# Optimization experiments

Hardware: AMD Instinct MI355X
Metric: run time of the kernel (lower is better)

Reference implementation:

```python
import jax, jax.numpy as jnp
import numpy as np

N_ATOMS = 2048
N_METAL = 512
BOX = (20.0, 20.0, 40.0)   # orthorhombic slab cell (A)
DL = 2.0                    # EwaldPotential dl -> k-grid half-extent per dim
SIGMA = 0.5540037           # 1/1.805132, Gaussian charge width
NMAX = tuple(int(np.ceil(L / DL)) for L in BOX)


def _kgrid():
    # integer reciprocal-lattice grid, k=0 excluded (built once at trace time)
    nx, ny, nz = NMAX
    g = np.stack(np.meshgrid(np.arange(-nx, nx + 1),
                             np.arange(-ny, ny + 1),
                             np.arange(-nz, nz + 1), indexing='ij'), -1).reshape(-1, 3)
    g = g[np.any(g != 0, axis=1)]
    return g.astype(np.float32)

_GRID = _kgrid()  # [K,3]


def ewald_field(r, q, cell):
    """Reciprocal-space Ewald potential phi_i = dE/dq_i for Gaussian-smeared charges.
    r:[N,3] q:[N,C] cell:[3,3] (rows = lattice vectors). Returns [N,C]."""
    V = jnp.abs(jnp.linalg.det(cell))
    recip = 2.0 * jnp.pi * jnp.linalg.inv(cell).T          # rows: reciprocal vectors
    k = jnp.asarray(_GRID, dtype=r.dtype) @ recip          # [K,3]
    k2 = jnp.sum(k * k, axis=-1)                           # [K]
    kfac = jnp.exp(-0.5 * SIGMA * SIGMA * k2) / k2         # exponent=1 kernel
    phase = r @ k.T                                        # [N,K]  (dominant traffic)
    c, s = jnp.cos(phase), jnp.sin(phase)
    cq = kfac[:, None] * (c.T @ q)                         # [K,C]
    sq = kfac[:, None] * (s.T @ q)
    return (4.0 * jnp.pi / V) * (c @ cq + s @ sq)          # [N,C]


def setup_inputs() -> dict:
    key = jax.random.key(0)
    k1, k2 = jax.random.split(key)
    box = jnp.asarray(BOX, dtype=jnp.float32)
    positions = jax.random.uniform(k1, (N_ATOMS, 3), dtype=jnp.float32) * box
    q = jax.random.normal(k2, (N_ATOMS, 1), dtype=jnp.float32) * 0.5
    cell = jnp.diag(box)
    # metal (Z=79) atoms occupy the first N_METAL slots; rest electrolyte (Z=8)
    atomic_numbers = jnp.concatenate([
        jnp.full((N_METAL,), 79, dtype=jnp.int32),
        jnp.full((N_ATOMS - N_METAL,), 8, dtype=jnp.int32)])
    return {"positions": positions, "q": q, "cell": cell,
            "atomic_numbers": atomic_numbers, "n_metal": N_METAL}


def reference(positions, q, cell, atomic_numbers, n_metal):
    nm = int(n_metal)  # static: metal atoms are the first nm rows
    dt = positions.dtype
    # q_all[metal] = 0
    q = q.at[:nm].set(0.0)
    # capacitance matrix S from detached coords (torch uses r.detach(), cell.detach())
    r_m = jax.lax.stop_gradient(positions[:nm])
    cell_d = jax.lax.stop_gradient(cell)
    A = ewald_field(r_m, jnp.eye(nm, dtype=dt), cell_d)     # [nm,nm] A_mat
    A_inv = jnp.linalg.inv(A)
    ones = jnp.ones((nm, 1), dtype=dt)
    Ai1 = A_inv @ ones                                       # [nm,1]
    S = A_inv - (Ai1 @ Ai1.T) / (ones.T @ Ai1)               # charge-neutral projector
    # full-system field; scaling_factor=1, external_field=None -> B_ext = 0
    f = ewald_field(positions, q, cell)                      # [N,1]
    B = -f[:nm]
    q_mw = q.at[:nm].set(S @ B)
    e_corr = jnp.zeros((1,), dtype=dt)   # scaling_factor == 1.0 branch
    e_ext = jnp.zeros((1,), dtype=dt)    # external_field is None
    return q_mw, e_corr, e_ext
```

## Files before the change

kernel.cpp:

```cpp
#include <hip/hip_runtime.h>
#include <math.h>

#define N_ATOMS 2048
#define NM      512
#define KHALF   9040
#define KPAD    9216
#define TWO_PI  6.2831853071795864769f
#define SIGMA   0.5540037f
#define FOUR_PI 12.566370614359172954f

__device__ inline void inv3x3(const float* __restrict__ c, float inv[3][3], float& det) {
    float a00=c[0],a01=c[1],a02=c[2],a10=c[3],a11=c[4],a12=c[5],a20=c[6],a21=c[7],a22=c[8];
    float c00 =  a11*a22 - a12*a21;
    float c01 = -(a10*a22 - a12*a20);
    float c02 =  a10*a21 - a11*a20;
    det = a00*c00 + a01*c01 + a02*c02;
    float id = 1.0f/det;
    inv[0][0] = c00*id;
    inv[0][1] = -(a01*a22 - a02*a21)*id;
    inv[0][2] =  (a01*a12 - a02*a11)*id;
    inv[1][0] = c01*id;
    inv[1][1] =  (a00*a22 - a02*a20)*id;
    inv[1][2] = -(a00*a12 - a02*a10)*id;
    inv[2][0] = c02*id;
    inv[2][1] = -(a00*a21 - a01*a20)*id;
    inv[2][2] =  (a00*a11 - a01*a10)*id;
}

__device__ __forceinline__ void gbar(int* cnt, int* flag, int ph, int G) {
    __syncthreads();
    if (threadIdx.x == 0) {
        __threadfence();
        int prev = __hip_atomic_fetch_add(cnt, 1, __ATOMIC_ACQ_REL, __HIP_MEMORY_SCOPE_AGENT);
        if (prev == G*ph - 1) {
            __hip_atomic_store(flag, ph, __ATOMIC_RELEASE, __HIP_MEMORY_SCOPE_AGENT);
        } else {
            while (__hip_atomic_load(flag, __ATOMIC_RELAXED, __HIP_MEMORY_SCOPE_AGENT) < ph)
                __builtin_amdgcn_s_sleep(4);
        }
        __threadfence();
    }
    __syncthreads();
}

__global__ void prep(const float* __restrict__ pos, const float* __restrict__ qv,
                     const float* __restrict__ cell, float4* __restrict__ kdata,
                     float4* __restrict__ uq, float* __restrict__ out) {
    const int bb = blockIdx.x, tid = threadIdx.x;
    if (bb < 36) {
        int t = bb*256 + tid;
        float gx=0.f, gy=0.f, gz=0.f, wk=0.f;
        if (t < KHALF) {
            int iz = t % 41; int rem = t / 41; int iy = rem % 21; int ix = rem / 21;
            gx = (float)(ix - 10); gy = (float)(iy - 10); gz = (float)(iz - 20);
            float inv[3][3], det;
            inv3x3(cell, inv, det);
            float kx = TWO_PI*(gx*inv[0][0] + gy*inv[0][1] + gz*inv[0][2]);
            float ky = TWO_PI*(gx*inv[1][0] + gy*inv[1][1] + gz*inv[1][2]);
            float kz = TWO_PI*(gx*inv[2][0] + gy*inv[2][1] + gz*inv[2][2]);
            float k2 = kx*kx + ky*ky + kz*kz;
            float kfac = __expf(-0.5f*SIGMA*SIGMA*k2) / k2;
            wk = sqrtf(2.0f*kfac);
        }
        kdata[t] = make_float4(gx, gy, gz, wk);
    } else {
        int i = (bb-36)*256 + tid;
        float inv[3][3], det;
        inv3x3(cell, inv, det);
        float x = pos[3*i], y = pos[3*i+1], z = pos[3*i+2];
        float u = x*inv[0][0] + y*inv[1][0] + z*inv[2][0];
        float v = x*inv[0][1] + y*inv[1][1] + z*inv[2][1];
        float w = x*inv[0][2] + y*inv[1][2] + z*inv[2][2];
        float qi = qv[i];
        uq[i] = make_float4(u, v, w, qi);
        if (i >= NM) out[i] = qi;
        if (i == 0) { out[N_ATOMS] = 0.f; out[N_ATOMS+1] = 0.f; }
    }
}

__global__ void __launch_bounds__(256, 2) syrk_sf(const float4* __restrict__ kdata,
        const float4* __restrict__ uq, float* __restrict__ partial,
        float* __restrict__ Scw, float* __restrict__ Ssw, int SL, int KSL, int nsyrk) {
    __shared__ float smem[16384];
    const int tid = threadIdx.x;
    if ((int)blockIdx.x >= nsyrk) {
        int ch = blockIdx.x - nsyrk;
        int kk = tid & 63, sp = tid >> 6;
        int k = ch*64 + kk;
        float4 kd = kdata[k];
        float sc = 0.f, ss = 0.f;
        int jlo = NM + sp*384, jhi = jlo + 384;
        for (int j = jlo; j < jhi; ++j) {
            float4 at = uq[j];
            float ph = TWO_PI*(kd.x*at.x + kd.y*at.y + kd.z*at.z);
            float s, c; __sincosf(ph, &s, &c);
            sc += at.w * c;
            ss += at.w * s;
        }
        smem[sp*64 + kk] = sc;
        smem[256 + sp*64 + kk] = ss;
        __syncthreads();
        if (sp == 0) {
            float c = smem[kk] + smem[64+kk] + smem[128+kk] + smem[192+kk];
            float s = smem[256+kk] + smem[320+kk] + smem[384+kk] + smem[448+kk];
            float kf2 = kd.w * kd.w;
            Scw[k] = kf2 * c;
            Ssw[k] = kf2 * s;
        }
        return;
    }
    int s = blockIdx.x % SL;
    int t = blockIdx.x / SL;
    int rt = 0;
    while ((rt+1)*(rt+2)/2 <= t) ++rt;
    int ct = t - rt*(rt+1)/2;
    const int row0 = rt << 7, c0 = ct << 7;
    const bool diag = (row0 == c0);
    float* crT = smem; float* srT = smem+4096; float* ccT = smem+8192; float* scT = smem+12288;
    const float* ccR = diag ? crT : ccT;
    const float* scR = diag ? srT : scT;
    const int i0 = (tid & 15) << 3;
    const int j0 = (tid >> 4) << 3;
    float acc[8][8];
    #pragma unroll
    for (int i = 0; i < 8; ++i)
        #pragma unroll
        for (int j = 0; j < 8; ++j) acc[i][j] = 0.f;
    const int k0 = s * KSL;
    const int nch = KSL >> 5;
    for (int ch = 0; ch < nch; ++ch) {
        int kc = k0 + (ch << 5);
        __syncthreads();
        #pragma unroll
        for (int w = 0; w < 16; ++w) {
            int job = tid + (w << 8);
            int kk = job >> 7, a = job & 127;
            float4 kd = kdata[kc + kk];
            float4 at = uq[row0 + a];
            float ph = TWO_PI*(kd.x*at.x + kd.y*at.y + kd.z*at.z);
            float sn, cs;
            __sincosf(ph, &sn, &cs);
            crT[kk*128+a] = kd.w * cs;
            srT[kk*128+a] = kd.w * sn;
        }
        if (!diag) {
            #pragma unroll
            for (int w = 0; w < 16; ++w) {
                int job = tid + (w << 8);
                int kk = job >> 7, a = job & 127;
                float4 kd = kdata[kc + kk];
                float4 at = uq[c0 + a];
                float ph = TWO_PI*(kd.x*at.x + kd.y*at.y + kd.z*at.z);
                float sn, cs;
                __sincosf(ph, &sn, &cs);
                ccT[kk*128+a] = kd.w * cs;
                scT[kk*128+a] = kd.w * sn;
            }
        }
        __syncthreads();
        #pragma unroll 4
        for (int kk = 0; kk < 32; ++kk) {
            float cr[8], sr[8], cc[8], sv[8];
            *(float4*)&cr[0] = *(const float4*)&crT[kk*128+i0];
            *(float4*)&cr[4] = *(const float4*)&crT[kk*128+i0+4];
            *(float4*)&sr[0] = *(const float4*)&srT[kk*128+i0];
            *(float4*)&sr[4] = *(const float4*)&srT[kk*128+i0+4];
            *(float4*)&cc[0] = *(const float4*)&ccR[kk*128+j0];
            *(float4*)&cc[4] = *(const float4*)&ccR[kk*128+j0+4];
            *(float4*)&sv[0] = *(const float4*)&scR[kk*128+j0];
            *(float4*)&sv[4] = *(const float4*)&scR[kk*128+j0+4];
            #pragma unroll
            for (int i = 0; i < 8; ++i)
                #pragma unroll
                for (int j = 0; j < 8; ++j)
                    acc[i][j] += cr[i]*cc[j] + sr[i]*sv[j];
        }
    }
    float* P = partial + ((size_t)blockIdx.x << 14);
    #pragma unroll
    for (int i = 0; i < 8; ++i) {
        *(float4*)&P[(i0+i)*128 + j0]     = make_float4(acc[i][0], acc[i][1], acc[i][2], acc[i][3]);
        *(float4*)&P[(i0+i)*128 + j0 + 4] = make_float4(acc[i][4], acc[i][5], acc[i][6], acc[i][7]);
    }
}

__device__ void diag_fast(float* D, float* T, float* M, int tid, int pd, float* Dinvs) {
    __syncthreads();
    if (tid < 64) {
        float row[64];
        #pragma unroll
        for (int c = 0; c < 64; ++c) row[c] = D[tid*68 + c];
        #pragma unroll
        for (int j = 0; j < 64; ++j) {
            float pj = __shfl(row[j], j);
            float rinv = 1.0f / sqrtf(pj);
            float lj = row[j] * rinv;
            row[j] = lj;
            #pragma unroll
            for (int c = j+1; c < 64; ++c) {
                float lcj = __shfl(lj, c);
                row[c] = fmaf(-lj, lcj, row[c]);
            }
        }
        #pragma unroll
        for (int c = 0; c < 64; ++c) D[tid*68 + c] = row[c];
    }
    __syncthreads();
    for (int idx = tid; idx < 64*68; idx += 256) T[idx] = 0.f;
    __syncthreads();
    if (tid < 64) {
        int s = tid >> 3, c = tid & 7, o = s*8;
        float x[8];
        #pragma unroll
        for (int r = 0; r < 8; ++r) {
            float acc = (r == c) ? 1.0f : 0.0f;
            #pragma unroll
            for (int j = 0; j < 8; ++j)
                if (j < r) acc -= D[(o+r)*68 + o + j] * x[j];
            x[r] = (r >= c) ? acc / D[(o+r)*68 + o + r] : 0.0f;
        }
        #pragma unroll
        for (int r = 0; r < 8; ++r)
            if (r >= c) T[(o+r)*68 + o + c] = x[r];
    }
    __syncthreads();
    #pragma unroll
    for (int lvl = 0; lvl < 3; ++lvl) {
        const int h = 8 << lvl, pairs = 4 >> lvl;
        const int hq = h >> 2, nq = pairs * h * hq;
        for (int e = tid; e < nq; e += 256) {
            int pr = e / (h*hq); int rem = e - pr*h*hq;
            int r2 = rem / hq, cq = rem - (rem/hq)*hq;
            int o = pr*2*h;
            float4 acc = make_float4(0.f, 0.f, 0.f, 0.f);
            for (int j2 = cq*4; j2 < h; ++j2) {
                float l = D[(o+h+r2)*68 + o + j2];
                float4 w = *(const float4*)&T[(o+j2)*68 + o + cq*4];
                acc.x += l*w.x; acc.y += l*w.y; acc.z += l*w.z; acc.w += l*w.w;
            }
            *(float4*)&M[(pr*h + r2)*h + cq*4] = acc;
        }
        __syncthreads();
        for (int e = tid; e < nq; e += 256) {
            int pr = e / (h*hq); int rem = e - pr*h*hq;
            int r2 = rem / hq, cq = rem - (rem/hq)*hq;
            int o = pr*2*h;
            float4 acc = make_float4(0.f, 0.f, 0.f, 0.f);
            for (int j2 = 0; j2 <= r2; ++j2) {
                float w = T[(o+h+r2)*68 + o+h + j2];
                float4 m = *(const float4*)&M[(pr*h + j2)*h + cq*4];
                acc.x += w*m.x; acc.y += w*m.y; acc.z += w*m.z; acc.w += w*m.w;
            }
            float4 st = make_float4(-acc.x, -acc.y, -acc.z, -acc.w);
            *(float4*)&T[(o+h+r2)*68 + o + cq*4] = st;
        }
        __syncthreads();
    }
    for (int idx = tid; idx < 4096; idx += 256) {
        int r = idx >> 6, c = idx & 63;
        Dinvs[pd*4096 + idx] = (c <= r) ? T[r*68+c] : 0.f;
    }
}

__global__ void __launch_bounds__(256) redfield(const float* __restrict__ partial,
        const float* __restrict__ cell, float* __restrict__ Amat,
        const float4* __restrict__ kdata, const float4* __restrict__ uq,
        const float* __restrict__ Scw, const float* __restrict__ Ssw,
        float* __restrict__ Bvec, int SL) {
    const int b = blockIdx.x, tid = threadIdx.x;
    float inv[3][3], det;
    inv3x3(cell, inv, det);
    const float scal = FOUR_PI / fabsf(det);
    if (b < 512) {
        for (int idx = b*256 + tid; idx < 512*512; idx += 512*256) {
            int i = idx >> 9, j = idx & 511;
            if (i < j) continue;
            int rt2 = i >> 7, ct2 = j >> 7;
            int t2 = rt2*(rt2+1)/2 + ct2;
            const float* p = partial + ((size_t)(t2*SL) << 14) + ((i & 127) << 7) + (j & 127);
            float a0=0.f,a1=0.f,a2=0.f,a3=0.f,a4=0.f,a5=0.f,a6=0.f,a7=0.f;
            int s = 0;
            for (; s + 8 <= SL; s += 8) {
                a0 += p[(size_t)(s+0) << 14];
                a1 += p[(size_t)(s+1) << 14];
                a2 += p[(size_t)(s+2) << 14];
                a3 += p[(size_t)(s+3) << 14];
                a4 += p[(size_t)(s+4) << 14];
                a5 += p[(size_t)(s+5) << 14];
                a6 += p[(size_t)(s+6) << 14];
                a7 += p[(size_t)(s+7) << 14];
            }
            for (; s < SL; ++s) a0 += p[(size_t)s << 14];
            float sum = ((a0+a1)+(a2+a3)) + ((a4+a5)+(a6+a7));
            float v = scal * sum;
            Amat[(size_t)i*512 + j] = v;
            Amat[(size_t)j*512 + i] = v;
        }
    } else {
        int ch = b - 512;
        int atom = ch*4 + (tid >> 6);
        int lane = tid & 63;
        float4 at = uq[atom];
        float acc = 0.f;
        for (int k = lane; k < KPAD; k += 64) {
            float4 kd = kdata[k];
            float ph = TWO_PI*(kd.x*at.x + kd.y*at.y + kd.z*at.z);
            float s, c; __sincosf(ph, &s, &c);
            acc += c*Scw[k] + s*Ssw[k];
        }
        #pragma unroll
        for (int off = 32; off; off >>= 1) acc += __shfl_down(acc, off);
        if (lane == 0) Bvec[atom] = -scal * acc;
    }
}

__global__ void __launch_bounds__(256) tail_persist(float* __restrict__ Amat,
        float* __restrict__ Lmat, float* __restrict__ LmatT, float* __restrict__ Dinvs,
        const float* __restrict__ Bvec, float* __restrict__ out,
        int* cnt, int* flag) {
    __shared__ float smem[15360];
    const int b = blockIdx.x, tid = threadIdx.x;
    const int G = 28;

    if (b == 0) {
        float* D = smem; float* T = smem + 4352; float* M = smem + 8704;
        for (int idx = tid; idx < 4096; idx += 256) {
            int r = idx >> 6, c = idx & 63;
            D[r*68+c] = Amat[(size_t)r*512 + c];
        }
        diag_fast(D, T, M, tid, 0, Dinvs);
    }
    gbar(cnt, flag, 1, G);

    for (int p = 0; p <= 6; ++p) {
        const int T7 = 7 - p, ntile = T7*(T7+1)/2;
        if (b < ntile) {
            const int tt = b;
            int rt = 0; while ((rt+1)*(rt+2)/2 <= tt) ++rt;
            const int ct = tt - rt*(rt+1)/2;
            const int R = p + 1 + rt, C = p + 1 + ct;
            float* ArT = smem;
            float* DvT = smem + 4352;
            float* LrT = smem + 8704;
            float* LcT = smem + 13056;
            float pref[16];
            if (R != C) {
                #pragma unroll
                for (int w = 0; w < 16; ++w) {
                    int idx = tid + (w << 8);
                    pref[w] = Amat[(size_t)(C*64 + (idx >> 6))*512 + p*64 + (idx & 63)];
                }
            }
            __syncthreads();
            for (int idx = tid; idx < 4096; idx += 256) {
                int j = idx >> 6, d = idx & 63;
                DvT[d*68 + j] = Dinvs[p*4096 + j*64 + d];
            }
            for (int idx = tid; idx < 4096; idx += 256) {
                int i = idx >> 6, k = idx & 63;
                ArT[k*68 + i] = Amat[(size_t)(R*64 + i)*512 + p*64 + k];
            }
            __syncthreads();
            const int i0 = (tid & 15)*4, j0 = (tid >> 4)*4;
            float lr[4][4];
            #pragma unroll
            for (int ii = 0; ii < 4; ++ii)
                #pragma unroll
                for (int jj = 0; jj < 4; ++jj) lr[ii][jj] = 0.f;
            for (int k = 0; k < 64; ++k) {
                float4 av = *(float4*)&ArT[k*68 + i0];
                float4 dv = *(float4*)&DvT[k*68 + j0];
                lr[0][0] += av.x*dv.x; lr[0][1] += av.x*dv.y; lr[0][2] += av.x*dv.z; lr[0][3] += av.x*dv.w;
                lr[1][0] += av.y*dv.x; lr[1][1] += av.y*dv.y; lr[1][2] += av.y*dv.z; lr[1][3] += av.y*dv.w;
                lr[2][0] += av.z*dv.x; lr[2][1] += av.z*dv.y; lr[2][2] += av.z*dv.z; lr[2][3] += av.z*dv.w;
                lr[3][0] += av.w*dv.x; lr[3][1] += av.w*dv.y; lr[3][2] += av.w*dv.z; lr[3][3] += av.w*dv.w;
            }
            #pragma unroll
            for (int ii = 0; ii < 4; ++ii)
                #pragma unroll
                for (int jj = 0; jj < 4; ++jj)
                    LrT[(j0+jj)*68 + i0+ii] = lr[ii][jj];
            __syncthreads();
            if (C == p + 1) {
                for (int idx = tid; idx < 4096; idx += 256) {
                    int i2 = idx >> 6, c2 = idx & 63;
                    Lmat[(size_t)(R*64+i2)*512 + p*64 + c2] = LrT[c2*68 + i2];
                }
                for (int idx = tid; idx < 4096; idx += 256) {
                    int c2 = idx >> 6, i2 = idx & 63;
                    LmatT[(size_t)(p*64+c2)*512 + R*64 + i2] = LrT[c2*68 + i2];
                }
            }
            if (R == C) {
                float up[4][4];
                #pragma unroll
                for (int ii = 0; ii < 4; ++ii)
                    #pragma unroll
                    for (int jj = 0; jj < 4; ++jj) up[ii][jj] = 0.f;
                for (int k = 0; k < 64; ++k) {
                    float4 av = *(float4*)&LrT[k*68 + i0];
                    float4 bv = *(float4*)&LrT[k*68 + j0];
                    up[0][0] += av.x*bv.x; up[0][1] += av.x*bv.y; up[0][2] += av.x*bv.z; up[0][3] += av.x*bv.w;
                    up[1][0] += av.y*bv.x; up[1][1] += av.y*bv.y; up[1][2] += av.y*bv.z; up[1][3] += av.y*bv.w;
                    up[2][0] += av.z*bv.x; up[2][1] += av.z*bv.y; up[2][2] += av.z*bv.z; up[2][3] += av.z*bv.w;
                    up[3][0] += av.w*bv.x; up[3][1] += av.w*bv.y; up[3][2] += av.w*bv.z; up[3][3] += av.w*bv.w;
                }
                float vals[4][4];
                #pragma unroll
                for (int ii = 0; ii < 4; ++ii)
                    #pragma unroll
                    for (int jj = 0; jj < 4; ++jj) {
                        size_t gix = (size_t)(R*64+i0+ii)*512 + C*64 + j0 + jj;
                        float v = Amat[gix] - up[ii][jj];
                        Amat[gix] = v;
                        vals[ii][jj] = v;
                    }
                if (tt == 0) {
                    float* D = smem; float* T = smem + 4352; float* M = smem + 8704;
                    __syncthreads();
                    #pragma unroll
                    for (int ii = 0; ii < 4; ++ii)
                        #pragma unroll
                        for (int jj = 0; jj < 4; ++jj)
                            D[(i0+ii)*68 + j0+jj] = vals[ii][jj];
                    diag_fast(D, T, M, tid, p+1, Dinvs);
                }
            } else {
                for (int w = 0; w < 16; ++w) {
                    int idx = tid + (w << 8);
                    ArT[(idx & 63)*68 + (idx >> 6)] = pref[w];
                }
                __syncthreads();
                const int c0l = (tid & 15)*4, jr0 = (tid >> 4)*2;
                #pragma unroll
                for (int hh = 0; hh < 2; ++hh) {
                    float lc[4][2];
                    #pragma unroll
                    for (int cc = 0; cc < 4; ++cc) { lc[cc][0] = 0.f; lc[cc][1] = 0.f; }
                    for (int d = 0; d < 64; ++d) {
                        float4 dv = *(float4*)&DvT[d*68 + c0l];
                        float2 av = *(float2*)&ArT[d*68 + hh*32 + jr0];
                        lc[0][0] += dv.x*av.x; lc[0][1] += dv.x*av.y;
                        lc[1][0] += dv.y*av.x; lc[1][1] += dv.y*av.y;
                        lc[2][0] += dv.z*av.x; lc[2][1] += dv.z*av.y;
                        lc[3][0] += dv.w*av.x; lc[3][1] += dv.w*av.y;
                    }
                    __syncthreads();
                    #pragma unroll
                    for (int cc = 0; cc < 4; ++cc) {
                        LcT[(c0l+cc)*36 + jr0]     = lc[cc][0];
                        LcT[(c0l+cc)*36 + jr0 + 1] = lc[cc][1];
                    }
                    __syncthreads();
                    float up[4][2];
                    #pragma unroll
                    for (int ii = 0; ii < 4; ++ii) { up[ii][0] = 0.f; up[ii][1] = 0.f; }
                    for (int c2 = 0; c2 < 64; ++c2) {
                        float4 lv = *(float4*)&LrT[c2*68 + i0];
                        float2 cv = *(float2*)&LcT[c2*36 + jr0];
                        up[0][0] += lv.x*cv.x; up[0][1] += lv.x*cv.y;
                        up[1][0] += lv.y*cv.x; up[1][1] += lv.y*cv.y;
                        up[2][0] += lv.z*cv.x; up[2][1] += lv.z*cv.y;
                        up[3][0] += lv.w*cv.x; up[3][1] += lv.w*cv.y;
                    }
                    #pragma unroll
                    for (int ii = 0; ii < 4; ++ii)
                        #pragma unroll
                        for (int jr = 0; jr < 2; ++jr) {
                            size_t gix = (size_t)(R*64+i0+ii)*512 + C*64 + hh*32 + jr0 + jr;
                            Amat[gix] -= up[ii][jr];
                        }
                }
            }
        }
        gbar(cnt, flag, p + 2, G);
    }

    if (b == 0) {
        float* rb  = smem;
        float* ro  = smem + 512;
        float* xb  = smem + 1024;
        float* xo  = smem + 1536;
        float* bvs = smem + 2048;
        float* red = smem + 2560;
        __syncthreads();
        for (int i = tid; i < 512; i += 256) {
            float bv = Bvec[i];
            bvs[i] = bv; rb[i] = bv; ro[i] = 1.0f;
        }
        __syncthreads();
        for (int k = 0; k < 8; ++k) {
            if (tid < 64) {
                const float* Dk = Dinvs + k*4096 + tid*64;
                float s1 = 0.f, s2 = 0.f;
                for (int c4 = 0; c4 < 16; ++c4) {
                    float4 w = *(const float4*)&Dk[c4*4];
                    int cb = 64*k + c4*4;
                    s1 += w.x*rb[cb] + w.y*rb[cb+1] + w.z*rb[cb+2] + w.w*rb[cb+3];
                    s2 += w.x*ro[cb] + w.y*ro[cb+1] + w.z*ro[cb+2] + w.w*ro[cb+3];
                }
                rb[64*k+tid] = s1; ro[64*k+tid] = s2;
            }
            __syncthreads();
            for (int mm = 64*(k+1) + tid; mm < 512; mm += 256) {
                const float* Lr = Lmat + (size_t)mm*512 + 64*k;
                float s1 = 0.f, s2 = 0.f;
                for (int c4 = 0; c4 < 16; ++c4) {
                    float4 l = *(const float4*)&Lr[c4*4];
                    int cb = 64*k + c4*4;
                    s1 += l.x*rb[cb] + l.y*rb[cb+1] + l.z*rb[cb+2] + l.w*rb[cb+3];
                    s2 += l.x*ro[cb] + l.y*ro[cb+1] + l.z*ro[cb+2] + l.w*ro[cb+3];
                }
                rb[mm] -= s1; ro[mm] -= s2;
            }
            __syncthreads();
        }
        for (int k = 7; k >= 0; --k) {
            if (tid < 64) {
                const float* D0 = Dinvs + k*4096;
                float s1 = 0.f, s2 = 0.f;
                for (int c = 0; c < 64; ++c) {
                    float w = D0[c*64 + tid];
                    s1 += w*rb[64*k+c]; s2 += w*ro[64*k+c];
                }
                xb[64*k+tid] = s1; xo[64*k+tid] = s2;
            }
            __syncthreads();
            for (int mm = tid; mm < 64*k; mm += 256) {
                const float* Ur = LmatT + (size_t)mm*512 + 64*k;
                float s1 = 0.f, s2 = 0.f;
                for (int c4 = 0; c4 < 16; ++c4) {
                    float4 u = *(const float4*)&Ur[c4*4];
                    int cb = 64*k + c4*4;
                    s1 += u.x*xb[cb] + u.y*xb[cb+1] + u.z*xb[cb+2] + u.w*xb[cb+3];
                    s2 += u.x*xo[cb] + u.y*xo[cb+1] + u.z*xo[cb+2] + u.w*xo[cb+3];
                }
                rb[mm] -= s1; ro[mm] -= s2;
            }
            __syncthreads();
        }
        float pn = 0.f, pd = 0.f;
        for (int i = tid; i < 512; i += 256) { pn += xo[i]*bvs[i]; pd += xo[i]; }
        #pragma unroll
        for (int off = 32; off; off >>= 1) { pn += __shfl_down(pn, off); pd += __shfl_down(pd, off); }
        if ((tid & 63) == 0) { red[tid >> 6] = pn; red[4 + (tid >> 6)] = pd; }
        __syncthreads();
        if (tid == 0) {
            float sn = red[0]+red[1]+red[2]+red[3];
            float sd = red[4]+red[5]+red[6]+red[7];
            red[8] = sn / sd;
        }
        __syncthreads();
        float ratio = red[8];
        for (int i = tid; i < 512; i += 256) out[i] = xb[i] - xo[i]*ratio;
    }
}

extern "C" void kernel_launch(void* const* d_in, const int* in_sizes, int n_in,
                              void* d_out, int out_size, void* d_ws, size_t ws_size,
                              hipStream_t stream) {
    (void)in_sizes; (void)n_in; (void)out_size;
    const float* pos  = (const float*)d_in[0];
    const float* qv   = (const float*)d_in[1];
    const float* cell = (const float*)d_in[2];
    float* out = (float*)d_out;
    char* ws = (char*)d_ws;
    size_t off = 0;
    auto alloc = [&](size_t bytes) -> void* {
        void* p = (void*)(ws + off);
        off = (off + bytes + 255) & ~(size_t)255;
        return p;
    };
    float4* kdata = (float4*)alloc((size_t)KPAD*16);
    float4* uq    = (float4*)alloc((size_t)N_ATOMS*16);
    float*  Scw   = (float*)alloc((size_t)KPAD*4);
    float*  Ssw   = (float*)alloc((size_t)KPAD*4);
    float*  Bvec  = (float*)alloc(512*4);
    float*  Amat  = (float*)alloc((size_t)512*512*4);
    float*  Lmat  = (float*)alloc((size_t)512*512*4);
    float*  LmatT = (float*)alloc((size_t)512*512*4);
    float*  Dinvs = (float*)alloc((size_t)8*4096*4);
    int* bar = (int*)alloc(256);
    static const int slopts[10] = {96, 72, 48, 36, 24, 16, 12, 8, 4, 1};
    int SL = 1;
    for (int ci = 0; ci < 10; ++ci) {
        size_t need = (size_t)10 * slopts[ci] * 16384 * 4;
        if (off + need <= ws_size) { SL = slopts[ci]; break; }
    }
    float* partial = (float*)alloc((size_t)10*SL*16384*4);
    const int KSL = KPAD / SL;
    const int nsyrk = 10*SL;

    hipMemsetAsync(bar, 0, 8, stream);
    prep<<<dim3(44), dim3(256), 0, stream>>>(pos, qv, cell, kdata, uq, out);
    syrk_sf<<<dim3(nsyrk + 144), dim3(256), 0, stream>>>(kdata, uq, partial,
                                                         Scw, Ssw, SL, KSL, nsyrk);
    redfield<<<dim3(640), dim3(256), 0, stream>>>(partial, cell, Amat, kdata, uq,
                                                  Scw, Ssw, Bvec, SL);
    tail_persist<<<dim3(28), dim3(256), 0, stream>>>(Amat, Lmat, LmatT, Dinvs,
                                                     Bvec, out, bar, bar + 1);
}
```

Baseline: 589.7 us.

## Split triangular solve into separate 512-thread kernel and vectorize tile loads

Moves the forward and back triangular solve out of the persistent Cholesky kernel into its own single-block, 512-thread kernel. The kernel boundary replaces the final grid barrier, and the doubled thread count halves the trailing-update loop trips. Tile loads of Amat and Dinvs into shared memory now use float4 global reads with transposed scalar stores. The grid barrier drops its explicit threadfences in favour of release/acquire atomics and polls with a shorter sleep. This adds one kernel launch and relies on the atomic ordering alone for correctness.

```diff
diff --git a/kernel.cpp b/kernel.cpp
--- a/kernel.cpp
+++ b/kernel.cpp
@@ -30,15 +30,15 @@
 __device__ __forceinline__ void gbar(int* cnt, int* flag, int ph, int G) {
     __syncthreads();
     if (threadIdx.x == 0) {
-        __threadfence();
-        int prev = __hip_atomic_fetch_add(cnt, 1, __ATOMIC_ACQ_REL, __HIP_MEMORY_SCOPE_AGENT);
+        int prev = __hip_atomic_fetch_add(cnt, 1, __ATOMIC_RELEASE, __HIP_MEMORY_SCOPE_AGENT);
         if (prev == G*ph - 1) {
+            (void)__hip_atomic_load(cnt, __ATOMIC_ACQUIRE, __HIP_MEMORY_SCOPE_AGENT);
             __hip_atomic_store(flag, ph, __ATOMIC_RELEASE, __HIP_MEMORY_SCOPE_AGENT);
         } else {
             while (__hip_atomic_load(flag, __ATOMIC_RELAXED, __HIP_MEMORY_SCOPE_AGENT) < ph)
-                __builtin_amdgcn_s_sleep(4);
-        }
-        __threadfence();
+                __builtin_amdgcn_s_sleep(2);
+            (void)__hip_atomic_load(flag, __ATOMIC_ACQUIRE, __HIP_MEMORY_SCOPE_AGENT);
+        }
     }
     __syncthreads();
 }
@@ -314,9 +314,8 @@
     }
 }
 
-__global__ void __launch_bounds__(256) tail_persist(float* __restrict__ Amat,
+__global__ void __launch_bounds__(256) tail_chol(float* __restrict__ Amat,
         float* __restrict__ Lmat, float* __restrict__ LmatT, float* __restrict__ Dinvs,
-        const float* __restrict__ Bvec, float* __restrict__ out,
         int* cnt, int* flag) {
     __shared__ float smem[15360];
     const int b = blockIdx.x, tid = threadIdx.x;
@@ -343,22 +342,34 @@
             float* DvT = smem + 4352;
             float* LrT = smem + 8704;
             float* LcT = smem + 13056;
-            float pref[16];
+            float4 pref4[4];
             if (R != C) {
                 #pragma unroll
-                for (int w = 0; w < 16; ++w) {
-                    int idx = tid + (w << 8);
-                    pref[w] = Amat[(size_t)(C*64 + (idx >> 6))*512 + p*64 + (idx & 63)];
+                for (int w = 0; w < 4; ++w) {
+                    int j = tid + (w << 8);
+                    pref4[w] = *(const float4*)&Amat[(size_t)(C*64 + (j >> 4))*512 + p*64 + (j & 15)*4];
                 }
             }
             __syncthreads();
-            for (int idx = tid; idx < 4096; idx += 256) {
-                int j = idx >> 6, d = idx & 63;
-                DvT[d*68 + j] = Dinvs[p*4096 + j*64 + d];
-            }
-            for (int idx = tid; idx < 4096; idx += 256) {
-                int i = idx >> 6, k = idx & 63;
-                ArT[k*68 + i] = Amat[(size_t)(R*64 + i)*512 + p*64 + k];
+            #pragma unroll
+            for (int w = 0; w < 4; ++w) {
+                int t4 = tid + (w << 8);
+                float4 v = *(const float4*)&Dinvs[p*4096 + t4*4];
+                int j = t4 >> 4, d0 = (t4 & 15)*4;
+                DvT[(d0+0)*68 + j] = v.x;
+                DvT[(d0+1)*68 + j] = v.y;
+                DvT[(d0+2)*68 + j] = v.z;
+                DvT[(d0+3)*68 + j] = v.w;
+            }
+            #pragma unroll
+            for (int w = 0; w < 4; ++w) {
+                int j = tid + (w << 8);
+                int i = j >> 4, k0 = (j & 15)*4;
+                float4 v = *(const float4*)&Amat[(size_t)(R*64 + i)*512 + p*64 + k0];
+                ArT[(k0+0)*68 + i] = v.x;
+                ArT[(k0+1)*68 + i] = v.y;
+                ArT[(k0+2)*68 + i] = v.z;
+                ArT[(k0+3)*68 + i] = v.w;
             }
             __syncthreads();
             const int i0 = (tid & 15)*4, j0 = (tid >> 4)*4;
@@ -426,9 +437,14 @@
                     diag_fast(D, T, M, tid, p+1, Dinvs);
                 }
             } else {
-                for (int w = 0; w < 16; ++w) {
-                    int idx = tid + (w << 8);
-                    ArT[(idx & 63)*68 + (idx >> 6)] = pref[w];
+                #pragma unroll
+                for (int w = 0; w < 4; ++w) {
+                    int j = tid + (w << 8);
+                    int i = j >> 4, k0 = (j & 15)*4;
+                    ArT[(k0+0)*68 + i] = pref4[w].x;
+                    ArT[(k0+1)*68 + i] = pref4[w].y;
+                    ArT[(k0+2)*68 + i] = pref4[w].z;
+                    ArT[(k0+3)*68 + i] = pref4[w].w;
                 }
                 __syncthreads();
                 const int c0l = (tid & 15)*4, jr0 = (tid >> 4)*2;
@@ -473,87 +489,91 @@
                 }
             }
         }
-        gbar(cnt, flag, p + 2, G);
-    }
-
-    if (b == 0) {
-        float* rb  = smem;
-        float* ro  = smem + 512;
-        float* xb  = smem + 1024;
-        float* xo  = smem + 1536;
-        float* bvs = smem + 2048;
-        float* red = smem + 2560;
-        __syncthreads();
-        for (int i = tid; i < 512; i += 256) {
-            float bv = Bvec[i];
-            bvs[i] = bv; rb[i] = bv; ro[i] = 1.0f;
-        }
-        __syncthreads();
-        for (int k = 0; k < 8; ++k) {
-            if (tid < 64) {
-                const float* Dk = Dinvs + k*4096 + tid*64;
-                float s1 = 0.f, s2 = 0.f;
-                for (int c4 = 0; c4 < 16; ++c4) {
-                    float4 w = *(const float4*)&Dk[c4*4];
-                    int cb = 64*k + c4*4;
-                    s1 += w.x*rb[cb] + w.y*rb[cb+1] + w.z*rb[cb+2] + w.w*rb[cb+3];
-                    s2 += w.x*ro[cb] + w.y*ro[cb+1] + w.z*ro[cb+2] + w.w*ro[cb+3];
-                }
-                rb[64*k+tid] = s1; ro[64*k+tid] = s2;
-            }
-            __syncthreads();
-            for (int mm = 64*(k+1) + tid; mm < 512; mm += 256) {
-                const float* Lr = Lmat + (size_t)mm*512 + 64*k;
-                float s1 = 0.f, s2 = 0.f;
-                for (int c4 = 0; c4 < 16; ++c4) {
-                    float4 l = *(const float4*)&Lr[c4*4];
-                    int cb = 64*k + c4*4;
-                    s1 += l.x*rb[cb] + l.y*rb[cb+1] + l.z*rb[cb+2] + l.w*rb[cb+3];
-                    s2 += l.x*ro[cb] + l.y*ro[cb+1] + l.z*ro[cb+2] + l.w*ro[cb+3];
-                }
-                rb[mm] -= s1; ro[mm] -= s2;
-            }
-            __syncthreads();
-        }
-        for (int k = 7; k >= 0; --k) {
-            if (tid < 64) {
-                const float* D0 = Dinvs + k*4096;
-                float s1 = 0.f, s2 = 0.f;
-                for (int c = 0; c < 64; ++c) {
-                    float w = D0[c*64 + tid];
-                    s1 += w*rb[64*k+c]; s2 += w*ro[64*k+c];
-                }
-                xb[64*k+tid] = s1; xo[64*k+tid] = s2;
-            }
-            __syncthreads();
-            for (int mm = tid; mm < 64*k; mm += 256) {
-                const float* Ur = LmatT + (size_t)mm*512 + 64*k;
-                float s1 = 0.f, s2 = 0.f;
-                for (int c4 = 0; c4 < 16; ++c4) {
-                    float4 u = *(const float4*)&Ur[c4*4];
-                    int cb = 64*k + c4*4;
-                    s1 += u.x*xb[cb] + u.y*xb[cb+1] + u.z*xb[cb+2] + u.w*xb[cb+3];
-                    s2 += u.x*xo[cb] + u.y*xo[cb+1] + u.z*xo[cb+2] + u.w*xo[cb+3];
-                }
-                rb[mm] -= s1; ro[mm] -= s2;
-            }
-            __syncthreads();
-        }
-        float pn = 0.f, pd = 0.f;
-        for (int i = tid; i < 512; i += 256) { pn += xo[i]*bvs[i]; pd += xo[i]; }
-        #pragma unroll
-        for (int off = 32; off; off >>= 1) { pn += __shfl_down(pn, off); pd += __shfl_down(pd, off); }
-        if ((tid & 63) == 0) { red[tid >> 6] = pn; red[4 + (tid >> 6)] = pd; }
-        __syncthreads();
-        if (tid == 0) {
-            float sn = red[0]+red[1]+red[2]+red[3];
-            float sd = red[4]+red[5]+red[6]+red[7];
-            red[8] = sn / sd;
-        }
-        __syncthreads();
-        float ratio = red[8];
-        for (int i = tid; i < 512; i += 256) out[i] = xb[i] - xo[i]*ratio;
-    }
+        if (p < 6) gbar(cnt, flag, p + 2, G);
+    }
+}
+
+__global__ void __launch_bounds__(512) solve(const float* __restrict__ Lmat,
+        const float* __restrict__ LmatT, const float* __restrict__ Dinvs,
+        const float* __restrict__ Bvec, float* __restrict__ out) {
+    __shared__ float smem[2592];
+    float* rb  = smem;
+    float* ro  = smem + 512;
+    float* xb  = smem + 1024;
+    float* xo  = smem + 1536;
+    float* bvs = smem + 2048;
+    float* red = smem + 2560;
+    const int tid = threadIdx.x;
+    if (tid < 512) {
+        float bv = Bvec[tid];
+        bvs[tid] = bv; rb[tid] = bv; ro[tid] = 1.0f;
+    }
+    __syncthreads();
+    for (int k = 0; k < 8; ++k) {
+        if (tid < 64) {
+            const float* Dk = Dinvs + k*4096 + tid*64;
+            float s1 = 0.f, s2 = 0.f;
+            for (int c4 = 0; c4 < 16; ++c4) {
+                float4 w = *(const float4*)&Dk[c4*4];
+                int cb = 64*k + c4*4;
+                s1 += w.x*rb[cb] + w.y*rb[cb+1] + w.z*rb[cb+2] + w.w*rb[cb+3];
+                s2 += w.x*ro[cb] + w.y*ro[cb+1] + w.z*ro[cb+2] + w.w*ro[cb+3];
+            }
+            rb[64*k+tid] = s1; ro[64*k+tid] = s2;
+        }
+        __syncthreads();
+        for (int mm = 64*(k+1) + tid; mm < 512; mm += 512) {
+            const float* Lr = Lmat + (size_t)mm*512 + 64*k;
+            float s1 = 0.f, s2 = 0.f;
+            for (int c4 = 0; c4 < 16; ++c4) {
+                float4 l = *(const float4*)&Lr[c4*4];
+                int cb = 64*k + c4*4;
+                s1 += l.x*rb[cb] + l.y*rb[cb+1] + l.z*rb[cb+2] + l.w*rb[cb+3];
+                s2 += l.x*ro[cb] + l.y*ro[cb+1] + l.z*ro[cb+2] + l.w*ro[cb+3];
+            }
+            rb[mm] -= s1; ro[mm] -= s2;
+        }
+        __syncthreads();
+    }
+    for (int k = 7; k >= 0; --k) {
+        if (tid < 64) {
+            const float* D0 = Dinvs + k*4096;
+            float s1 = 0.f, s2 = 0.f;
+            for (int c = 0; c < 64; ++c) {
+                float w = D0[c*64 + tid];
+                s1 += w*rb[64*k+c]; s2 += w*ro[64*k+c];
+            }
+            xb[64*k+tid] = s1; xo[64*k+tid] = s2;
+        }
+        __syncthreads();
+        for (int mm = tid; mm < 64*k; mm += 512) {
+            const float* Ur = LmatT + (size_t)mm*512 + 64*k;
+            float s1 = 0.f, s2 = 0.f;
+            for (int c4 = 0; c4 < 16; ++c4) {
+                float4 u = *(const float4*)&Ur[c4*4];
+                int cb = 64*k + c4*4;
+                s1 += u.x*xb[cb] + u.y*xb[cb+1] + u.z*xb[cb+2] + u.w*xb[cb+3];
+                s2 += u.x*xo[cb] + u.y*xo[cb+1] + u.z*xo[cb+2] + u.w*xo[cb+3];
+            }
+            rb[mm] -= s1; ro[mm] -= s2;
+        }
+        __syncthreads();
+    }
+    float pn = 0.f, pd = 0.f;
+    if (tid < 512) { pn = xo[tid]*bvs[tid]; pd = xo[tid]; }
+    #pragma unroll
+    for (int off = 32; off; off >>= 1) { pn += __shfl_down(pn, off); pd += __shfl_down(pd, off); }
+    if ((tid & 63) == 0) { red[tid >> 6] = pn; red[16 + (tid >> 6)] = pd; }
+    __syncthreads();
+    if (tid == 0) {
+        float sn = 0.f, sd = 0.f;
+        #pragma unroll
+        for (int i = 0; i < 8; ++i) { sn += red[i]; sd += red[16+i]; }
+        red[31] = sn / sd;
+    }
+    __syncthreads();
+    float ratio = red[31];
+    if (tid < 512) out[tid] = xb[tid] - xo[tid]*ratio;
 }
 
 extern "C" void kernel_launch(void* const* d_in, const int* in_sizes, int n_in,
@@ -597,6 +617,7 @@
                                                          Scw, Ssw, SL, KSL, nsyrk);
     redfield<<<dim3(640), dim3(256), 0, stream>>>(partial, cell, Amat, kdata, uq,
                                                   Scw, Ssw, Bvec, SL);
-    tail_persist<<<dim3(28), dim3(256), 0, stream>>>(Amat, Lmat, LmatT, Dinvs,
-                                                     Bvec, out, bar, bar + 1);
-}
+    tail_chol<<<dim3(28), dim3(256), 0, stream>>>(Amat, Lmat, LmatT, Dinvs,
+                                                  bar, bar + 1);
+    solve<<<dim3(1), dim3(512), 0, stream>>>(Lmat, LmatT, Dinvs, Bvec, out);
+}
```

New measurement: 537.5 us. 8.9% less time.
